# Optimization experiments

Hardware: AMD Instinct MI355X
Metric: run time of the kernel (lower is better)

The kernel has to match this reference:

```python
import jax, jax.numpy as jnp
import numpy as np
import math

NUM_BUCKETS = 32
MAX_DISTANCE = 128
N_HEADS = 16
D_KV = 64
ATTN_SCALE = True


def _relative_position_bucket(relative_position, num_buckets=NUM_BUCKETS, max_distance=MAX_DISTANCE):
    # bidirectional (encoder) variant
    nb = num_buckets // 2
    buckets = (relative_position > 0).astype(jnp.int32) * nb
    rp = jnp.abs(relative_position)
    max_exact = nb // 2
    is_small = rp < max_exact
    rp_large = max_exact + (
        jnp.log(rp.astype(jnp.float32) / max_exact)
        / math.log(max_distance / max_exact)
        * (nb - max_exact)
    ).astype(jnp.int32)
    rp_large = jnp.minimum(rp_large, nb - 1)
    buckets = buckets + jnp.where(is_small, rp, rp_large)
    return buckets


def compute_bias(rel_bias_emb, q_len, k_len):
    ctx = jnp.arange(q_len)[:, None]
    mem = jnp.arange(k_len)[None, :]
    bucket = _relative_position_bucket(mem - ctx)  # [q,k] int32 in [0,32)
    values = rel_bias_emb[bucket]                  # [q,k,H]
    return jnp.transpose(values, (2, 0, 1))[None]  # [1,H,q,k]


def setup_inputs() -> dict:
    key = jax.random.key(0)
    k1, k2, k3, k4 = jax.random.split(key, 4)
    B, S, D = 2, 2048, 1024
    return {
        "hidden_states": jax.random.normal(k1, (B, S, D), jnp.float32),
        "attention_mask": jnp.ones((B, 1, S, S), jnp.float32),
        "W_qkv": jax.random.normal(k2, (D, 3 * D), jnp.float32) * 0.02,
        "W_o": jax.random.normal(k3, (D, D), jnp.float32) * 0.02,
        "rel_bias_emb": jax.random.normal(k4, (NUM_BUCKETS, N_HEADS), jnp.float32) * 0.02,
    }


def reference(hidden_states, attention_mask, W_qkv, W_o, rel_bias_emb):
    B, S, D = hidden_states.shape
    # fused QKV projection (no bias), then split as in split_tensor_along_last_dim
    qkv = jnp.einsum("bsd,de->bse", hidden_states, W_qkv)
    q, k, v = jnp.split(qkv, 3, axis=-1)
    # [b,s,H*d] -> [b,H,s,d]
    def to_heads(t):
        return jnp.transpose(t.reshape(B, S, N_HEADS, D_KV), (0, 2, 1, 3))
    q, k, v = to_heads(q), to_heads(k), to_heads(v)
    scores = jnp.einsum("bhqd,bhkd->bhqk", q, k)
    if ATTN_SCALE:
        scores = scores / math.sqrt(D_KV)
    position_bias = compute_bias(rel_bias_emb, S, S)  # [1,H,S,S]
    scores = scores * attention_mask + (-10000.0 * (1.0 - attention_mask) + position_bias)
    probs = jax.nn.softmax(scores, axis=-1)  # dropout = eval mode (identity)
    ctx = jnp.einsum("bhqk,bhkd->bhqd", probs, v)
    ctx = jnp.transpose(ctx, (0, 2, 1, 3)).reshape(B, S, N_HEADS * D_KV)
    attn_output = jnp.einsum("bse,ed->bsd", ctx, W_o)
    return attn_output
```

## Files before the change

### kernel.cpp

```cpp
#include <hip/hip_runtime.h>
#include <cstdint>

#define DEV static __device__ __forceinline__

typedef __bf16 bf16x8 __attribute__((ext_vector_type(8)));
typedef __bf16 bf16x4 __attribute__((ext_vector_type(4)));
typedef short  s16x4  __attribute__((ext_vector_type(4)));
typedef float  f32x4  __attribute__((ext_vector_type(4)));

DEV unsigned short f32_bf16(float f) {
  union { float f; unsigned u; } v; v.f = f;
  unsigned r = v.u + 0x7FFFu + ((v.u >> 16) & 1u);
  return (unsigned short)(r >> 16);
}

DEV void gload16(const void* g, void* lds) {
  __builtin_amdgcn_global_load_lds((__attribute__((address_space(1))) void*)g,
                                   (__attribute__((address_space(3))) void*)lds,
                                   16, 0, 0);
}

DEV float bcast_lane(float v, int srclane) {
  union { float f; int i; } u; u.f = v;
  u.i = __builtin_amdgcn_ds_bpermute(srclane << 2, u.i);
  return u.f;
}

DEV f32x4 mfma16_bf16(bf16x4 a, bf16x4 b, f32x4 c) {
  union { bf16x4 h; s16x4 s; } ua, ub; ua.h = a; ub.h = b;
#if __has_builtin(__builtin_amdgcn_mfma_f32_16x16x16bf16_1k)
  return __builtin_amdgcn_mfma_f32_16x16x16bf16_1k(ua.s, ub.s, c, 0, 0, 0);
#else
  f32x4 d;
  asm("v_mfma_f32_16x16x16_bf16 %0, %1, %2, %3" : "=v"(d) : "v"(ua.s), "v"(ub.s), "v"(c));
  return d;
#endif
}

__global__ void cast_bf16(const float* __restrict__ x, unsigned short* __restrict__ y) {
  int i = blockIdx.x * 256 + threadIdx.x;
  float4 v = ((const float4*)x)[i];
  uint2 o;
  o.x = (unsigned)f32_bf16(v.x) | ((unsigned)f32_bf16(v.y) << 16);
  o.y = (unsigned)f32_bf16(v.z) | ((unsigned)f32_bf16(v.w) << 16);
  ((uint2*)y)[i] = o;
}

__global__ void transpose_cast(const float* __restrict__ W, unsigned short* __restrict__ WT,
                               int K, int N) {
  __shared__ float t[64][65];
  int k0 = blockIdx.x * 64, n0 = blockIdx.y * 64;
  int tn = threadIdx.x & 63, tk = threadIdx.x >> 6;
#pragma unroll
  for (int i = 0; i < 64; i += 4)
    t[tk + i][tn] = W[(size_t)(k0 + tk + i) * N + n0 + tn];
  __syncthreads();
  int k2 = (threadIdx.x & 31) * 2, n = threadIdx.x >> 5;
#pragma unroll
  for (int i = 0; i < 64; i += 8) {
    int nn = n + i;
    unsigned o = (unsigned)f32_bf16(t[k2][nn]) | ((unsigned)f32_bf16(t[k2 + 1][nn]) << 16);
    *(unsigned*)&WT[(size_t)(n0 + nn) * K + k0 + k2] = o;
  }
}

__global__ void mask_check(const float* __restrict__ m, int* __restrict__ flag) {
  size_t i = ((size_t)blockIdx.x * 256 + threadIdx.x) * 4;
  float4 v = *(const float4*)(m + i);
  if (v.x != 1.0f || v.y != 1.0f || v.z != 1.0f || v.w != 1.0f) atomicOr(flag, 1);
}

template <int MODE, int TN>
__global__ void __launch_bounds__(256) gemm_bt(const unsigned short* __restrict__ A,
                                               const unsigned short* __restrict__ BT,
                                               float* __restrict__ Cout,
                                               unsigned short* __restrict__ Qb,
                                               unsigned short* __restrict__ Kb,
                                               unsigned short* __restrict__ VTb,
                                               int M, int N, int K) {
  constexpr int NT = TN / 32;
  __shared__ __align__(16) unsigned short As[128 * 32];
  __shared__ __align__(16) unsigned short Bs[TN * 32];
  const int tid = threadIdx.x, wave = tid >> 6, lane = tid & 63;
  const int l = lane & 15, quad = lane >> 4;
  const int wm = (wave & 1) * 64, wn = (wave >> 1) * (TN >> 1);
  const int bm = blockIdx.x, bn = blockIdx.y;

  const int srowA = wave * 32 + (lane >> 2);
  const int sswzA = ((lane & 3) ^ (srowA & 3)) * 8;
  const int srowB = (TN == 128) ? srowA : (wave * 16 + (lane >> 2));
  const int sswzB = ((lane & 3) ^ (srowB & 3)) * 8;
  const unsigned short* pA = A + (size_t)(bm * 128 + srowA) * K + sswzA;
  const unsigned short* pB = BT + (size_t)(bn * TN + srowB) * K + sswzB;
  unsigned short* ldsA0 = &As[(wave * 32) * 32];
  unsigned short* ldsA1 = &As[(wave * 32 + 16) * 32];
  unsigned short* ldsB0 = &Bs[((TN == 128 ? wave * 32 : wave * 16)) * 32];
  unsigned short* ldsB1 = &Bs[(wave * 32 + 16) * 32];

  f32x4 acc[4][NT];
#pragma unroll
  for (int i = 0; i < 4; i++)
#pragma unroll
    for (int j = 0; j < NT; j++) { f32x4 z = {0.f, 0.f, 0.f, 0.f}; acc[i][j] = z; }

  for (int kt = 0; kt < K; kt += 32) {
    __syncthreads();
    gload16(pA, ldsA0);
    gload16(pA + (size_t)16 * K, ldsA1);
    gload16(pB, ldsB0);
    if (TN == 128) gload16(pB + (size_t)16 * K, ldsB1);
    pA += 32; pB += 32;
    __syncthreads();
    bf16x8 af[4], bv[NT];
#pragma unroll
    for (int mt = 0; mt < 4; mt++) {
      int r = wm + mt * 16 + l;
      af[mt] = *(const bf16x8*)&As[r * 32 + ((quad ^ (r & 3)) * 8)];
    }
#pragma unroll
    for (int nt = 0; nt < NT; nt++) {
      int r = wn + nt * 16 + l;
      bv[nt] = *(const bf16x8*)&Bs[r * 32 + ((quad ^ (r & 3)) * 8)];
    }
#pragma unroll
    for (int mt = 0; mt < 4; mt++)
#pragma unroll
      for (int nt = 0; nt < NT; nt++)
        acc[mt][nt] = __builtin_amdgcn_mfma_f32_16x16x32_bf16(af[mt], bv[nt], acc[mt][nt], 0, 0, 0);
  }

#pragma unroll
  for (int nt = 0; nt < NT; nt++) {
    const int col = bn * TN + wn + nt * 16 + l;
#pragma unroll
    for (int mt = 0; mt < 4; mt++) {
      const int row0 = bm * 128 + wm + mt * 16 + quad * 4;
      if (MODE == 0) {
#pragma unroll
        for (int r = 0; r < 4; r++)
          Cout[(size_t)(row0 + r) * N + col] = acc[mt][nt][r];
      } else {
        const int bb = row0 >> 11, s = row0 & 2047;
        if (col < 2048) {
          unsigned short* dst = (col < 1024) ? Qb : Kb;
          const int c = col & 1023;
          const size_t off = ((size_t)(bb * 16 + (c >> 6)) * 2048 + s) * 64 + (c & 63);
#pragma unroll
          for (int r = 0; r < 4; r++)
            dst[off + (size_t)r * 64] = f32_bf16(acc[mt][nt][r]);
        } else {
          const int c = col - 2048;
          const size_t off = ((size_t)(bb * 16 + (c >> 6)) * 64 + (c & 63)) * 2048 + s;
          bf16x4 pk;
#pragma unroll
          for (int r = 0; r < 4; r++) pk[r] = (__bf16)acc[mt][nt][r];
          *(bf16x4*)&VTb[off] = pk;
        }
      }
    }
  }
}

__global__ void __launch_bounds__(256, 2) attn(const unsigned short* __restrict__ Qb,
                                               const unsigned short* __restrict__ Kb,
                                               const unsigned short* __restrict__ VTb,
                                               const float* __restrict__ mask,
                                               const float* __restrict__ emb,
                                               const int* __restrict__ mflag,
                                               unsigned short* __restrict__ ctx) {
  __shared__ __align__(16) unsigned short Ks[128 * 64];
  __shared__ __align__(16) unsigned short VTs[64 * 128];
  __shared__ float biasLUT[512];

  const float LOG2E = 1.4426950408889634f;
  const float c1 = 0.125f * LOG2E;
  const float C2 = 10000.0f * LOG2E;
  const int tid = threadIdx.x, wave = tid >> 6, lane = tid & 63;
  const int l = lane & 15, quad = lane >> 4;
  const int qt = blockIdx.x & 15, bh = blockIdx.x >> 4;
  const int b = bh >> 4, h = bh & 15;
  const int q0 = qt * 128;

  for (int i = tid; i < 512; i += 256) {
    int rel = i - 256;
    int rp = rel < 0 ? -rel : rel;
    int off = rp < 8 ? rp
                     : 8 + (rp >= 12) + (rp >= 16) + (rp >= 23) + (rp >= 32) +
                           (rp >= 46) + (rp >= 64) + (rp >= 91);
    int bucket = (rel > 0 ? 16 : 0) + off;
    biasLUT[i] = emb[bucket * 16 + h] * LOG2E;
  }
  const float satL = emb[15 * 16 + h] * LOG2E;
  const float satH = emb[31 * 16 + h] * LOG2E;
  const int masked = *mflag;

  const unsigned short* qb  = Qb  + ((size_t)(b * 16 + h) * 2048 + q0) * 64;
  const unsigned short* kb  = Kb  + (size_t)(b * 16 + h) * 2048 * 64;
  const unsigned short* vtb = VTb + (size_t)(b * 16 + h) * 64 * 2048;
  const float* mbase = mask + (size_t)b * 2048 * 2048;

  {
    const int rw = lane >> 3, c = lane & 7;
#pragma unroll
    for (int j = 0; j < 4; j++) {
      int row = wave * 32 + j * 8 + rw;
      gload16(qb + (size_t)row * 64 + ((c ^ (row & 7)) * 8), &Ks[(wave * 32 + j * 8) * 64]);
    }
  }
  __syncthreads();
  bf16x8 qf[2][2];
#pragma unroll
  for (int mtq = 0; mtq < 2; mtq++)
#pragma unroll
    for (int ks = 0; ks < 2; ks++) {
      int row = wave * 32 + mtq * 16 + l;
      qf[mtq][ks] = *(const bf16x8*)&Ks[row * 64 + (((ks * 4 + quad) ^ (row & 7)) * 8)];
    }

  float lr[2] = {0.f, 0.f};
  f32x4 Oa[2][4];
#pragma unroll
  for (int mt = 0; mt < 2; mt++)
#pragma unroll
    for (int dt = 0; dt < 4; dt++) { f32x4 z = {0.f, 0.f, 0.f, 0.f}; Oa[mt][dt] = z; }

  for (int kt = 0; kt < 16; kt++) {
    const int k0 = kt * 128;
    __syncthreads();
    {
      const int rw = lane >> 3, c = lane & 7;
#pragma unroll
      for (int j = 0; j < 4; j++) {
        int row = wave * 32 + j * 8 + rw;
        gload16(kb + (size_t)(k0 + row) * 64 + ((c ^ (row & 7)) * 8),
                &Ks[(wave * 32 + j * 8) * 64]);
      }
    }
    {
      const int rw = lane >> 4, c = lane & 15;
#pragma unroll
      for (int j = 0; j < 4; j++) {
        int drow = wave * 16 + j * 4 + rw;
        gload16(vtb + (size_t)drow * 2048 + k0 + ((c ^ (drow & 7)) * 8),
                &VTs[(wave * 16 + j * 4) * 128]);
      }
    }
    __syncthreads();

    const int d0 = k0 - q0;
    const bool sat = (d0 >= 256) || (d0 <= -256);
    const float bias_u = d0 > 0 ? satH : satL;
    const int ibase = 256 + d0 + quad * 4 - wave * 32 - l;
    bf16x4 pa[2][8];

#pragma unroll
    for (int ntk = 0; ntk < 8; ntk++) {
      int row = ntk * 16 + l;
      bf16x8 kf0 = *(const bf16x8*)&Ks[row * 64 + ((quad ^ (row & 7)) * 8)];
      bf16x8 kf1 = *(const bf16x8*)&Ks[row * 64 + (((4 + quad) ^ (row & 7)) * 8)];
#pragma unroll
      for (int mtq = 0; mtq < 2; mtq++) {
        f32x4 s = {0.f, 0.f, 0.f, 0.f};
        s = __builtin_amdgcn_mfma_f32_16x16x32_bf16(kf0, qf[mtq][0], s, 0, 0, 0);
        s = __builtin_amdgcn_mfma_f32_16x16x32_bf16(kf1, qf[mtq][1], s, 0, 0, 0);

        const int ib = ibase - mtq * 16 + ntk * 16;
        if (!masked) {
          if (sat) {
#pragma unroll
            for (int r = 0; r < 4; r++) s[r] = fmaf(s[r], c1, bias_u);
          } else {
#pragma unroll
            for (int r = 0; r < 4; r++) s[r] = fmaf(s[r], c1, biasLUT[ib + r]);
          }
        } else {
          const int qg = q0 + wave * 32 + mtq * 16 + l;
          const int kg = k0 + ntk * 16 + quad * 4;
          float4 mv4 = *(const float4*)&mbase[(size_t)qg * 2048 + kg];
#pragma unroll
          for (int r = 0; r < 4; r++) {
            float mv = r == 0 ? mv4.x : (r == 1 ? mv4.y : (r == 2 ? mv4.z : mv4.w));
            float bias = sat ? bias_u : biasLUT[ib + r];
            s[r] = fmaf(s[r], mv * c1, fmaf(mv, C2, bias - C2));
          }
        }
        bf16x4 pk;
        float ls = 0.f;
#pragma unroll
        for (int r = 0; r < 4; r++) {
          float p = __builtin_amdgcn_exp2f(fminf(s[r], 30.0f));
          ls += p;
          pk[r] = (__bf16)p;
        }
        lr[mtq] += ls;
        pa[mtq][ntk] = pk;
      }
    }

#pragma unroll
    for (int ntk = 0; ntk < 8; ntk++) {
      bf16x4 vf[4];
#pragma unroll
      for (int dt = 0; dt < 4; dt++) {
        int row = dt * 16 + l;
        int ch = (ntk * 2 + (quad >> 1)) ^ (l & 7);
        vf[dt] = *(const bf16x4*)&VTs[row * 128 + ch * 8 + (quad & 1) * 4];
      }
#pragma unroll
      for (int mtq = 0; mtq < 2; mtq++)
#pragma unroll
        for (int dt = 0; dt < 4; dt++)
          Oa[mtq][dt] = mfma16_bf16(pa[mtq][ntk], vf[dt], Oa[mtq][dt]);
    }
  }

  float inv[2];
#pragma unroll
  for (int mtq = 0; mtq < 2; mtq++) {
    float v = lr[mtq];
    v += __shfl_xor(v, 16);
    v += __shfl_xor(v, 32);
    inv[mtq] = 1.0f / v;
  }
#pragma unroll
  for (int mt = 0; mt < 2; mt++)
#pragma unroll
    for (int r = 0; r < 4; r++) {
      float i_bc = bcast_lane(inv[mt], quad * 4 + r);
      const int qg = q0 + wave * 32 + mt * 16 + quad * 4 + r;
#pragma unroll
      for (int dt = 0; dt < 4; dt++)
        ctx[(size_t)(b * 2048 + qg) * 1024 + h * 64 + dt * 16 + l] =
            f32_bf16(Oa[mt][dt][r] * i_bc);
    }
}

extern "C" void kernel_launch(void* const* d_in, const int* in_sizes, int n_in,
                              void* d_out, int out_size, void* d_ws, size_t ws_size,
                              hipStream_t stream) {
  const float* hs   = (const float*)d_in[0];
  const float* mask = (const float*)d_in[1];
  const float* wqkv = (const float*)d_in[2];
  const float* wo   = (const float*)d_in[3];
  const float* emb  = (const float*)d_in[4];
  float* out = (float*)d_out;

  char* ws = (char*)d_ws;
  unsigned short* hB  = (unsigned short*)(ws);
  unsigned short* ctx = (unsigned short*)(ws);
  unsigned short* wqT = (unsigned short*)(ws + 8388608);
  unsigned short* woT = (unsigned short*)(ws + 14680064);
  unsigned short* Qb  = (unsigned short*)(ws + 16777216);
  unsigned short* Kb  = (unsigned short*)(ws + 25165824);
  unsigned short* VTb = (unsigned short*)(ws + 33554432);
  int* mflag          = (int*)(ws + 41943040);
  if (ws_size < 41943044) return;

  hipMemsetAsync(mflag, 0, 4, stream);
  cast_bf16<<<4096, 256, 0, stream>>>(hs, hB);
  transpose_cast<<<dim3(16, 48), 256, 0, stream>>>(wqkv, wqT, 1024, 3072);
  transpose_cast<<<dim3(16, 16), 256, 0, stream>>>(wo, woT, 1024, 1024);
  mask_check<<<8192, 256, 0, stream>>>(mask, mflag);
  gemm_bt<2, 128><<<dim3(32, 24), 256, 0, stream>>>(hB, wqT, nullptr, Qb, Kb, VTb, 4096, 3072, 1024);
  attn<<<512, 256, 0, stream>>>(Qb, Kb, VTb, mask, emb, mflag, ctx);
  gemm_bt<0, 64><<<dim3(32, 16), 256, 0, stream>>>(ctx, woT, out, nullptr, nullptr, nullptr, 4096, 1024, 1024);
}
```

Measured before the change: 235.1 us.

## Double-buffer K/V tiles in LDS with two-tile-ahead prefetch

Replaces the single K and V^T LDS tiles with two ping-pong buffers. The first two key tiles are loaded up front, and the loads for tile kt+2 are issued after tile kt's compute. This removes the per-iteration load-then-barrier stall at the top of the loop, so global-to-LDS traffic can overlap with MFMA and softmax work. It also drops the fminf clamp before exp2, which removes an overflow guard on the unnormalized scores. The cost is doubled LDS use per block, and it relies on the end-of-iteration barrier draining outstanding loads.

Result: faster. 225.2 us (-4.2%).

```diff
diff --git a/kernel.cpp b/kernel.cpp
--- a/kernel.cpp
+++ b/kernel.cpp
@@ -168,8 +168,7 @@
                                                const float* __restrict__ emb,
                                                const int* __restrict__ mflag,
                                                unsigned short* __restrict__ ctx) {
-  __shared__ __align__(16) unsigned short Ks[128 * 64];
-  __shared__ __align__(16) unsigned short VTs[64 * 128];
+  __shared__ __align__(16) unsigned short KV[2][16384];
   __shared__ float biasLUT[512];
 
   const float LOG2E = 1.4426950408889634f;
@@ -199,23 +198,49 @@
   const unsigned short* vtb = VTb + (size_t)(b * 16 + h) * 64 * 2048;
   const float* mbase = mask + (size_t)b * 2048 * 2048;
 
-  {
-    const int rw = lane >> 3, c = lane & 7;
-#pragma unroll
-    for (int j = 0; j < 4; j++) {
-      int row = wave * 32 + j * 8 + rw;
-      gload16(qb + (size_t)row * 64 + ((c ^ (row & 7)) * 8), &Ks[(wave * 32 + j * 8) * 64]);
-    }
+  const int rw8 = lane >> 3, c8 = lane & 7;
+  const int rw16 = lane >> 4, c16 = lane & 15;
+
+#pragma unroll
+  for (int j = 0; j < 4; j++) {
+    int row = wave * 32 + j * 8 + rw8;
+    gload16(qb + (size_t)row * 64 + ((c8 ^ (row & 7)) * 8), &KV[1][(wave * 32 + j * 8) * 64]);
+  }
+#pragma unroll
+  for (int j = 0; j < 4; j++) {
+    int row = wave * 32 + j * 8 + rw8;
+    gload16(kb + (size_t)row * 64 + ((c8 ^ (row & 7)) * 8), &KV[0][(wave * 32 + j * 8) * 64]);
+  }
+#pragma unroll
+  for (int j = 0; j < 4; j++) {
+    int drow = wave * 16 + j * 4 + rw16;
+    gload16(vtb + (size_t)drow * 2048 + ((c16 ^ (drow & 7)) * 8),
+            &KV[0][8192 + (wave * 16 + j * 4) * 128]);
   }
   __syncthreads();
+
   bf16x8 qf[2][2];
 #pragma unroll
   for (int mtq = 0; mtq < 2; mtq++)
 #pragma unroll
     for (int ks = 0; ks < 2; ks++) {
       int row = wave * 32 + mtq * 16 + l;
-      qf[mtq][ks] = *(const bf16x8*)&Ks[row * 64 + (((ks * 4 + quad) ^ (row & 7)) * 8)];
-    }
+      qf[mtq][ks] = *(const bf16x8*)&KV[1][row * 64 + (((ks * 4 + quad) ^ (row & 7)) * 8)];
+    }
+  __syncthreads();
+
+#pragma unroll
+  for (int j = 0; j < 4; j++) {
+    int row = wave * 32 + j * 8 + rw8;
+    gload16(kb + (size_t)(128 + row) * 64 + ((c8 ^ (row & 7)) * 8),
+            &KV[1][(wave * 32 + j * 8) * 64]);
+  }
+#pragma unroll
+  for (int j = 0; j < 4; j++) {
+    int drow = wave * 16 + j * 4 + rw16;
+    gload16(vtb + (size_t)drow * 2048 + 128 + ((c16 ^ (drow & 7)) * 8),
+            &KV[1][8192 + (wave * 16 + j * 4) * 128]);
+  }
 
   float lr[2] = {0.f, 0.f};
   f32x4 Oa[2][4];
@@ -226,26 +251,8 @@
 
   for (int kt = 0; kt < 16; kt++) {
     const int k0 = kt * 128;
-    __syncthreads();
-    {
-      const int rw = lane >> 3, c = lane & 7;
-#pragma unroll
-      for (int j = 0; j < 4; j++) {
-        int row = wave * 32 + j * 8 + rw;
-        gload16(kb + (size_t)(k0 + row) * 64 + ((c ^ (row & 7)) * 8),
-                &Ks[(wave * 32 + j * 8) * 64]);
-      }
-    }
-    {
-      const int rw = lane >> 4, c = lane & 15;
-#pragma unroll
-      for (int j = 0; j < 4; j++) {
-        int drow = wave * 16 + j * 4 + rw;
-        gload16(vtb + (size_t)drow * 2048 + k0 + ((c ^ (drow & 7)) * 8),
-                &VTs[(wave * 16 + j * 4) * 128]);
-      }
-    }
-    __syncthreads();
+    const unsigned short* Ks  = KV[kt & 1];
+    const unsigned short* VTs = KV[kt & 1] + 8192;
 
     const int d0 = k0 - q0;
     const bool sat = (d0 >= 256) || (d0 <= -256);
@@ -288,7 +295,7 @@
         float ls = 0.f;
 #pragma unroll
         for (int r = 0; r < 4; r++) {
-          float p = __builtin_amdgcn_exp2f(fminf(s[r], 30.0f));
+          float p = __builtin_amdgcn_exp2f(s[r]);
           ls += p;
           pk[r] = (__bf16)p;
         }
@@ -311,6 +318,24 @@
 #pragma unroll
         for (int dt = 0; dt < 4; dt++)
           Oa[mtq][dt] = mfma16_bf16(pa[mtq][ntk], vf[dt], Oa[mtq][dt]);
+    }
+
+    __syncthreads();
+    if (kt + 2 < 16) {
+      const int kn = (kt + 2) * 128;
+      unsigned short* dst = (unsigned short*)KV[kt & 1];
+#pragma unroll
+      for (int j = 0; j < 4; j++) {
+        int row = wave * 32 + j * 8 + rw8;
+        gload16(kb + (size_t)(kn + row) * 64 + ((c8 ^ (row & 7)) * 8),
+                &dst[(wave * 32 + j * 8) * 64]);
+      }
+#pragma unroll
+      for (int j = 0; j < 4; j++) {
+        int drow = wave * 16 + j * 4 + rw16;
+        gload16(vtb + (size_t)drow * 2048 + kn + ((c16 ^ (drow & 7)) * 8),
+                &dst[8192 + (wave * 16 + j * 4) * 128]);
+      }
     }
   }
 
```
